# Kernel tuning notes

Hardware: AMD Instinct MI355X
Metric: run time of the kernel (lower is better)

The kernel has to match this reference:

```python
import jax, jax.numpy as jnp
import numpy as np

B = 32768      # batch
D = 2          # input_dim
H = 2048       # hidden_dim
NQ = 4         # qubits


def setup_inputs() -> dict:
    key = jax.random.key(0)
    ks = jax.random.split(key, 14)

    def lin(k, fan_in, fan_out):
        # kaiming-uniform-ish init like nn.Linear
        bound = 1.0 / np.sqrt(fan_in)
        kw, kb = jax.random.split(k)
        W = jax.random.uniform(kw, (fan_in, fan_out), jnp.float32, -bound, bound)
        b = jax.random.uniform(kb, (fan_out,), jnp.float32, -bound, bound)
        return W, b

    x = jax.random.normal(ks[0], (B, D), jnp.float32)
    W1, b1 = lin(ks[1], D + NQ, H)      # core Linear 1
    W2, b2 = lin(ks[2], H, H)           # core Linear 2
    Wc, bc = lin(ks[3], H, 1)           # classifier
    Wr1, br1 = lin(ks[4], D, 8)
    Wr2, br2 = lin(ks[5], 8, 4)
    Wr3, br3 = lin(ks[6], 4, 1)
    return dict(x=x, W1=W1, b1=b1, W2=W2, b2=b2, Wc=Wc, bc=bc,
                Wr1=Wr1, br1=br1, Wr2=Wr2, br2=br2, Wr3=Wr3, br3=br3)


def _quantum_feature_map(x):
    # Exact closed form of: RY(x_i) on 4 qubits from |0000>, CNOT(0,1), CNOT(2,3),
    # expval(PauliZ(i)). Padding with zeros -> cos(0)=1 on unused wires.
    xq = jnp.pad(x, ((0, 0), (0, NQ - x.shape[1])))  # [B,4]
    c = jnp.cos(xq)
    return jnp.stack([c[:, 0], c[:, 0] * c[:, 1], c[:, 2], c[:, 2] * c[:, 3]], axis=1)


def reference(x, W1, b1, W2, b2, Wc, bc, Wr1, br1, Wr2, br2, Wr3, br3):
    qfeat = _quantum_feature_map(x)               # [B,4]
    concat = jnp.concatenate([x, qfeat], axis=1)  # [B, D+4]
    h = jnp.tanh(concat @ W1 + b1)                # [B,H]
    h = jnp.tanh(h @ W2 + b2)                     # [B,H]
    logits = h @ Wc + bc                          # [B,1]
    r = jnp.tanh(x @ Wr1 + br1)
    r = jnp.tanh(r @ Wr2 + br2)
    risk = r @ Wr3 + br3                          # [B,1]
    return logits, risk
```

## Files before the change

### kernel.cpp

```cpp
#include <hip/hip_runtime.h>
#include <hip/hip_bf16.h>
#include <stdint.h>

#define B_ROWS 32768
#define HID    2048
#define K_DIM  2048

#define BM 128
#define BN 256
#define NKT 16

#define SCALE_W   5747.3639f
#define DEQUANT   1.3700225e-6f

#define L1_BLOCKS (B_ROWS / 32)
#define TR_BLOCKS ((HID/32)*(K_DIM/32))

typedef int  int4v __attribute__((ext_vector_type(4)));
typedef char char8 __attribute__((ext_vector_type(8)));


__device__ __forceinline__ float fast_tanh(float x) {
    float e = __expf(2.0f * x);
    return 1.0f - 2.0f * __builtin_amdgcn_rcpf(e + 1.0f);
}

#define SCHED_FENCE() __builtin_amdgcn_sched_barrier(0)

__device__ __forceinline__ const char* uniform_ptr(const char* p) {
    uint64_t v = (uint64_t)(uintptr_t)p;
    uint32_t lo = __builtin_amdgcn_readfirstlane((uint32_t)v);
    uint32_t hi = __builtin_amdgcn_readfirstlane((uint32_t)(v >> 32));
    return (const char*)(uintptr_t)(((uint64_t)hi << 32) | lo);
}

__global__ __launch_bounds__(256) void prep_kernel(
    const float* __restrict__ x,   const float* __restrict__ W1, const float* __restrict__ b1,
    const float* __restrict__ W2,
    const float* __restrict__ Wr1, const float* __restrict__ br1,
    const float* __restrict__ Wr2, const float* __restrict__ br2,
    const float* __restrict__ Wr3, const float* __restrict__ br3,
    const float* __restrict__ bc,
    char* __restrict__ h1, char* __restrict__ W2t, float* __restrict__ out) {
    const int t = threadIdx.x;
    if (blockIdx.x >= L1_BLOCKS) {
        __shared__ float tile[32][33];
        const int tb = blockIdx.x - L1_BLOCKS;
        const int n0 = (tb & 63) * 32;
        const int k0 = (tb >> 6) * 32;
        const int tx = t & 31;
        const int ty = t >> 5;
#pragma unroll
        for (int i = 0; i < 4; ++i) {
            int k = k0 + ty + i * 8;
            tile[ty + i * 8][tx] = W2[(size_t)k * HID + n0 + tx];
        }
        __syncthreads();
        if (t < 64) {
            const int n    = n0 + (t & 31);
            const int lkq  = t >> 5;
            const int kq64 = ((k0 >> 4) + lkq) & 3;
            int w[4];
#pragma unroll
            for (int q = 0; q < 4; ++q) {
                int v = 0;
#pragma unroll
                for (int j = 0; j < 4; ++j) {
                    int c = __float2int_rn(tile[lkq * 16 + q * 4 + j][n - n0] * SCALE_W) & 255;
                    v |= c << (8 * j);
                }
                w[q] = v;
            }
            char* dst = W2t + ((size_t)(n >> 4) * 32 + (k0 >> 6)) * 1024
                      + ((n & 15) + (kq64 << 4)) * 16;
            *(int4v*)dst = int4v{w[0], w[1], w[2], w[3]};
        }
        return;
    }
    __shared__ float4 xsh[32];
    const int brow0 = blockIdx.x * 32;
    if (t < 32) {
        const float2 xv = *(const float2*)(x + 2 * (brow0 + t));
        const float c0 = __cosf(xv.x);
        xsh[t] = float4{xv.x, xv.y, c0, c0 * __cosf(xv.y)};
    }
    const int n0 = t * 8;
    float w0[8], w1[8], w2[8], w3[8], wb[8];
#pragma unroll
    for (int j = 0; j < 8; ++j) {
        w0[j] = W1[0 * HID + n0 + j];
        w1[j] = W1[1 * HID + n0 + j];
        w2[j] = W1[2 * HID + n0 + j];
        w3[j] = W1[3 * HID + n0 + j];
        wb[j] = W1[4 * HID + n0 + j] + W1[5 * HID + n0 + j] + b1[n0 + j];
    }
    const size_t kblk = (size_t)(n0 >> 6);
    const int    kq   = (n0 >> 4) & 3;
    const int    bofs = n0 & 15;
    __syncthreads();
#pragma unroll 2
    for (int r = 0; r < 32; ++r) {
        const float4 xr = xsh[r];
        char8 v;
#pragma unroll
        for (int j = 0; j < 8; ++j) {
            float z = wb[j] + xr.x * w0[j] + xr.y * w1[j] + xr.z * w2[j] + xr.w * w3[j];
            v[j] = (char)__float2int_rn(fast_tanh(z) * 127.0f);
        }
        const int row = brow0 + r;
        char* dst = h1 + ((size_t)(row >> 4) * 32 + kblk) * 1024
                  + ((row & 15) + (kq << 4)) * 16 + bofs;
        *(char8*)dst = v;
    }
    if (t < 32) {
        const float x0 = xsh[t].x, x1 = xsh[t].y;
        float r1[8];
#pragma unroll
        for (int j = 0; j < 8; ++j)
            r1[j] = fast_tanh(br1[j] + x0 * Wr1[j] + x1 * Wr1[8 + j]);
        float r2[4];
#pragma unroll
        for (int j = 0; j < 4; ++j) {
            float s = br2[j];
#pragma unroll
            for (int i = 0; i < 8; ++i) s += r1[i] * Wr2[i * 4 + j];
            r2[j] = fast_tanh(s);
        }
        float risk = br3[0];
#pragma unroll
        for (int i = 0; i < 4; ++i) risk += r2[i] * Wr3[i];
        out[B_ROWS + brow0 + t] = risk;
        out[brow0 + t]          = bc[0];
    }
}

__global__ __launch_bounds__(256, 2) void gemm_kernel(
    const char* __restrict__ A,
    const char* __restrict__ Bt,
    const float* __restrict__ b2, const float* __restrict__ Wc,
    float* __restrict__ out) {
    const int tid  = threadIdx.x;
    const int wave = tid >> 6;
    const int lane = tid & 63;
    const int bid  = blockIdx.x;
    const int m0 = (bid >> 3) * BM;
    const int n0 = (bid & 7) * BN;

    const int mw   = (wave & 1) * 64;
    const int nw   = (wave >> 1) * 128;
    const int quad = lane >> 4;
    const int r16  = lane & 15;

    const char* aB = uniform_ptr(A  + (size_t)((m0 + mw) >> 4) * 32768);
    const char* bB = uniform_ptr(Bt + (size_t)((n0 + nw) >> 4) * 32768);
    uint32_t voA[4], voB[8];
#pragma unroll
    for (int mi = 0; mi < 4; ++mi) voA[mi] = lane * 16 + mi * 32768;
#pragma unroll
    for (int ni = 0; ni < 8; ++ni) voB[ni] = lane * 16 + ni * 32768;

    int4v acc[4][8] = {};
    int4v a0[4], a1[4], b0[8], b1[8];

#pragma unroll
    for (int mi = 0; mi < 4; ++mi) a0[mi] = *(const int4v*)(aB + voA[mi]);
#pragma unroll
    for (int ni = 0; ni < 8; ++ni) b0[ni] = *(const int4v*)(bB + voB[ni]);

    for (int u = 0; u < NKT; ++u) {
#pragma unroll
        for (int mi = 0; mi < 4; ++mi) a1[mi] = *(const int4v*)(aB + voA[mi] + 1024);
#pragma unroll
        for (int ni = 0; ni < 8; ++ni) b1[ni] = *(const int4v*)(bB + voB[ni] + 1024);
        SCHED_FENCE();
#pragma unroll
        for (int mi = 0; mi < 4; ++mi)
#pragma unroll
            for (int ni = 0; ni < 8; ++ni)
                acc[mi][ni] = __builtin_amdgcn_mfma_i32_16x16x64_i8(
                    a0[mi], b0[ni], acc[mi][ni], 0, 0, 0);
        if (u + 1 < NKT) {
#pragma unroll
            for (int mi = 0; mi < 4; ++mi) {
                voA[mi] += 2048;
                a0[mi] = *(const int4v*)(aB + voA[mi]);
            }
#pragma unroll
            for (int ni = 0; ni < 8; ++ni) {
                voB[ni] += 2048;
                b0[ni] = *(const int4v*)(bB + voB[ni]);
            }
        }
        SCHED_FENCE();
#pragma unroll
        for (int mi = 0; mi < 4; ++mi)
#pragma unroll
            for (int ni = 0; ni < 8; ++ni)
                acc[mi][ni] = __builtin_amdgcn_mfma_i32_16x16x64_i8(
                    a1[mi], b1[ni], acc[mi][ni], 0, 0, 0);
    }

    float b2v[8], wcv[8];
#pragma unroll
    for (int ni = 0; ni < 8; ++ni) {
        int gn = n0 + nw + ni * 16 + r16;
        b2v[ni] = b2[gn];
        wcv[ni] = Wc[gn];
    }
#pragma unroll
    for (int mi = 0; mi < 4; ++mi) {
#pragma unroll
        for (int r = 0; r < 4; ++r) {
            int gm = m0 + mw + mi * 16 + quad * 4 + r;
            float rs = 0.f;
#pragma unroll
            for (int ni = 0; ni < 8; ++ni)
                rs += fast_tanh((float)acc[mi][ni][r] * DEQUANT + b2v[ni]) * wcv[ni];
            rs += __shfl_xor(rs, 1);
            rs += __shfl_xor(rs, 2);
            rs += __shfl_xor(rs, 4);
            rs += __shfl_xor(rs, 8);
            if (r16 == 0) atomicAdd(&out[gm], rs);
        }
    }
}

extern "C" void kernel_launch(void* const* d_in, const int* in_sizes, int n_in,
                              void* d_out, int out_size, void* d_ws, size_t ws_size,
                              hipStream_t stream) {
    const float* x   = (const float*)d_in[0];
    const float* W1  = (const float*)d_in[1];
    const float* b1  = (const float*)d_in[2];
    const float* W2  = (const float*)d_in[3];
    const float* b2  = (const float*)d_in[4];
    const float* Wc  = (const float*)d_in[5];
    const float* bc  = (const float*)d_in[6];
    const float* Wr1 = (const float*)d_in[7];
    const float* br1 = (const float*)d_in[8];
    const float* Wr2 = (const float*)d_in[9];
    const float* br2 = (const float*)d_in[10];
    const float* Wr3 = (const float*)d_in[11];
    const float* br3 = (const float*)d_in[12];
    float* out = (float*)d_out;

    char* W2t = (char*)d_ws;
    char* h1  = (char*)d_ws + (size_t)4 * 1024 * 1024;

    prep_kernel<<<L1_BLOCKS + TR_BLOCKS, 256, 0, stream>>>(
        x, W1, b1, W2, Wr1, br1, Wr2, br2, Wr3, br3, bc, h1, W2t, out);
    gemm_kernel<<<(B_ROWS / BM) * (HID / BN), 256, 0, stream>>>(h1, W2t, b2, Wc, out);
}
```

Measured before the change: 253.8 us.

## Restructure prep kernel: full-16B layer-1 stores, 64x64 transpose tiles, separate regressor blocks

```diff
diff --git a/kernel.cpp b/kernel.cpp
--- a/kernel.cpp
+++ b/kernel.cpp
@@ -13,11 +13,11 @@
 #define SCALE_W   5747.3639f
 #define DEQUANT   1.3700225e-6f
 
-#define L1_BLOCKS (B_ROWS / 32)
-#define TR_BLOCKS ((HID/32)*(K_DIM/32))
+#define L1B 512
+#define TRB 1024
+#define RGB 128
 
 typedef int  int4v __attribute__((ext_vector_type(4)));
-typedef char char8 __attribute__((ext_vector_type(8)));
 
 
 __device__ __forceinline__ float fast_tanh(float x) {
@@ -42,78 +42,53 @@
     const float* __restrict__ Wr3, const float* __restrict__ br3,
     const float* __restrict__ bc,
     char* __restrict__ h1, char* __restrict__ W2t, float* __restrict__ out) {
-    const int t = threadIdx.x;
-    if (blockIdx.x >= L1_BLOCKS) {
-        __shared__ float tile[32][33];
-        const int tb = blockIdx.x - L1_BLOCKS;
-        const int n0 = (tb & 63) * 32;
-        const int k0 = (tb >> 6) * 32;
-        const int tx = t & 31;
-        const int ty = t >> 5;
-#pragma unroll
-        for (int i = 0; i < 4; ++i) {
-            int k = k0 + ty + i * 8;
-            tile[ty + i * 8][tx] = W2[(size_t)k * HID + n0 + tx];
-        }
-        __syncthreads();
-        if (t < 64) {
-            const int n    = n0 + (t & 31);
-            const int lkq  = t >> 5;
-            const int kq64 = ((k0 >> 4) + lkq) & 3;
-            int w[4];
+    const int t   = threadIdx.x;
+    const int bid = blockIdx.x;
+
+    if (bid < L1B) {
+        const int wave = t >> 6, lane = t & 63;
+        const int W = bid * 4 + wave;
+        const int kb = W & 31;
+        const int r0 = (W >> 5) * 512;
+        const int c0 = kb * 64 + ((lane >> 4) << 4);
+        float w0[16], w1[16], w2[16], w3[16], wb[16];
+#pragma unroll
+        for (int j = 0; j < 16; ++j) {
+            w0[j] = W1[0 * HID + c0 + j];
+            w1[j] = W1[1 * HID + c0 + j];
+            w2[j] = W1[2 * HID + c0 + j];
+            w3[j] = W1[3 * HID + c0 + j];
+            wb[j] = W1[4 * HID + c0 + j] + W1[5 * HID + c0 + j] + b1[c0 + j];
+        }
+        const int lr = lane & 15;
+        char* dbase = h1 + (size_t)((r0 >> 4) * 32 + kb) * 1024 + lane * 16;
+        for (int it = 0; it < 32; ++it) {
+            const int row = r0 + it * 16 + lr;
+            const float2 xv = *(const float2*)(x + 2 * row);
+            const float c0f = __cosf(xv.x);
+            const float cc  = c0f * __cosf(xv.y);
+            int wpk[4];
 #pragma unroll
             for (int q = 0; q < 4; ++q) {
                 int v = 0;
 #pragma unroll
-                for (int j = 0; j < 4; ++j) {
-                    int c = __float2int_rn(tile[lkq * 16 + q * 4 + j][n - n0] * SCALE_W) & 255;
-                    v |= c << (8 * j);
+                for (int jj = 0; jj < 4; ++jj) {
+                    const int j = q * 4 + jj;
+                    float z = wb[j] + xv.x * w0[j] + xv.y * w1[j]
+                                    + c0f * w2[j] + cc * w3[j];
+                    v |= (__float2int_rn(fast_tanh(z) * 127.0f) & 255) << (8 * jj);
                 }
-                w[q] = v;
+                wpk[q] = v;
             }
-            char* dst = W2t + ((size_t)(n >> 4) * 32 + (k0 >> 6)) * 1024
-                      + ((n & 15) + (kq64 << 4)) * 16;
-            *(int4v*)dst = int4v{w[0], w[1], w[2], w[3]};
+            *(int4v*)(dbase + (size_t)it * 32 * 1024) = int4v{wpk[0], wpk[1], wpk[2], wpk[3]};
         }
         return;
     }
-    __shared__ float4 xsh[32];
-    const int brow0 = blockIdx.x * 32;
-    if (t < 32) {
-        const float2 xv = *(const float2*)(x + 2 * (brow0 + t));
-        const float c0 = __cosf(xv.x);
-        xsh[t] = float4{xv.x, xv.y, c0, c0 * __cosf(xv.y)};
-    }
-    const int n0 = t * 8;
-    float w0[8], w1[8], w2[8], w3[8], wb[8];
-#pragma unroll
-    for (int j = 0; j < 8; ++j) {
-        w0[j] = W1[0 * HID + n0 + j];
-        w1[j] = W1[1 * HID + n0 + j];
-        w2[j] = W1[2 * HID + n0 + j];
-        w3[j] = W1[3 * HID + n0 + j];
-        wb[j] = W1[4 * HID + n0 + j] + W1[5 * HID + n0 + j] + b1[n0 + j];
-    }
-    const size_t kblk = (size_t)(n0 >> 6);
-    const int    kq   = (n0 >> 4) & 3;
-    const int    bofs = n0 & 15;
-    __syncthreads();
-#pragma unroll 2
-    for (int r = 0; r < 32; ++r) {
-        const float4 xr = xsh[r];
-        char8 v;
-#pragma unroll
-        for (int j = 0; j < 8; ++j) {
-            float z = wb[j] + xr.x * w0[j] + xr.y * w1[j] + xr.z * w2[j] + xr.w * w3[j];
-            v[j] = (char)__float2int_rn(fast_tanh(z) * 127.0f);
-        }
-        const int row = brow0 + r;
-        char* dst = h1 + ((size_t)(row >> 4) * 32 + kblk) * 1024
-                  + ((row & 15) + (kq << 4)) * 16 + bofs;
-        *(char8*)dst = v;
-    }
-    if (t < 32) {
-        const float x0 = xsh[t].x, x1 = xsh[t].y;
+
+    if (bid >= L1B + TRB) {
+        const int row = (bid - (L1B + TRB)) * 256 + t;
+        const float2 xv = *(const float2*)(x + 2 * row);
+        const float x0 = xv.x, x1 = xv.y;
         float r1[8];
 #pragma unroll
         for (int j = 0; j < 8; ++j)
@@ -129,9 +104,43 @@
         float risk = br3[0];
 #pragma unroll
         for (int i = 0; i < 4; ++i) risk += r2[i] * Wr3[i];
-        out[B_ROWS + brow0 + t] = risk;
-        out[brow0 + t]          = bc[0];
-    }
+        out[B_ROWS + row] = risk;
+        out[row]          = bc[0];
+        return;
+    }
+
+    const int tb = bid - L1B;
+    const int kt = tb >> 5;
+    const int nt = tb & 31;
+    const int k0 = kt * 64, n0 = nt * 64;
+    __shared__ float tile[64][65];
+#pragma unroll
+    for (int i = 0; i < 4; ++i) {
+        const int kl = i * 16 + (t >> 4);
+        const int cj = (t & 15) * 4;
+        const float4 v = *(const float4*)(W2 + (size_t)(k0 + kl) * HID + n0 + cj);
+        tile[kl][cj]     = v.x;
+        tile[kl][cj + 1] = v.y;
+        tile[kl][cj + 2] = v.z;
+        tile[kl][cj + 3] = v.w;
+    }
+    __syncthreads();
+    const int nl = ((t >> 6) << 4) + (t & 15);
+    const int kc = (t >> 4) & 3;
+    const int n  = n0 + nl;
+    int wpk[4];
+#pragma unroll
+    for (int q = 0; q < 4; ++q) {
+        int v = 0;
+#pragma unroll
+        for (int jj = 0; jj < 4; ++jj) {
+            int c = __float2int_rn(tile[kc * 16 + q * 4 + jj][nl] * SCALE_W) & 255;
+            v |= c << (8 * jj);
+        }
+        wpk[q] = v;
+    }
+    char* dst = W2t + (size_t)((n >> 4) * 32 + kt) * 1024 + ((n & 15) + kc * 16) * 16;
+    *(int4v*)dst = int4v{wpk[0], wpk[1], wpk[2], wpk[3]};
 }
 
 __global__ __launch_bounds__(256, 2) void gemm_kernel(
@@ -246,7 +255,7 @@
     char* W2t = (char*)d_ws;
     char* h1  = (char*)d_ws + (size_t)4 * 1024 * 1024;
 
-    prep_kernel<<<L1_BLOCKS + TR_BLOCKS, 256, 0, stream>>>(
+    prep_kernel<<<L1B + TRB + RGB, 256, 0, stream>>>(
         x, W1, b1, W2, Wr1, br1, Wr2, br2, Wr3, br3, bc, h1, W2t, out);
     gemm_kernel<<<(B_ROWS / BM) * (HID / BN), 256, 0, stream>>>(h1, W2t, b2, Wc, out);
 }
```

Measured after the change: 258.9 us. +2.0%, slower.
